# Kernel tuning notes

Measured on AMD Instinct MI355X. Metric: run time of the kernel, lower is better.

Reference implementation:

```python
import jax, jax.numpy as jnp
import numpy as np

B, T, D = 2, 2048, 2048
H = 16
HD = D // H  # 128


def _rotate_half(x):
    x1, x2 = x[..., :HD // 2], x[..., HD // 2:]
    return jnp.concatenate((-x2, x1), axis=-1)


def setup_inputs() -> dict:
    key = jax.random.key(0)
    ks = jax.random.split(key, 7)
    return {
        "x": jax.random.normal(ks[0], (B, T, D), dtype=jnp.float32),
        "rope_cos": jax.random.uniform(ks[1], (1, 1, T, HD), dtype=jnp.float32),
        "rope_sin": jax.random.uniform(ks[2], (1, 1, T, HD), dtype=jnp.float32),
        "qkv_w": jax.random.normal(ks[3], (3 * D, D), dtype=jnp.float32) * (1.0 / np.sqrt(D)),
        "qkv_b": jax.random.normal(ks[4], (3 * D,), dtype=jnp.float32) * 0.02,
        "out_w": jax.random.normal(ks[5], (D, D), dtype=jnp.float32) * (1.0 / np.sqrt(D)),
        "out_b": jax.random.normal(ks[6], (D,), dtype=jnp.float32) * 0.02,
    }


def reference(x, rope_cos, rope_sin, qkv_w, qkv_b, out_w, out_b):
    bsz, t, d = x.shape
    # fused QKV projection (torch Linear: x @ W.T + b)
    qkv = x @ qkv_w.T + qkv_b                       # [B, T, 3D]
    qkv = qkv.reshape(bsz, t, 3, H, HD).transpose(2, 0, 3, 1, 4)  # [3, B, H, T, HD]
    q, k, v = qkv[0], qkv[1], qkv[2]
    # RoPE
    cos = rope_cos[:, :, :t, :]
    sin = rope_sin[:, :, :t, :]
    q = q * cos + _rotate_half(q) * sin
    k = k * cos + _rotate_half(k) * sin
    # causal SDPA (eval mode -> no dropout)
    scale = 1.0 / np.sqrt(HD)
    scores = jnp.einsum("bhqd,bhkd->bhqk", q, k) * scale
    causal = jnp.tril(jnp.ones((t, t), dtype=bool))
    scores = jnp.where(causal, scores, jnp.finfo(scores.dtype).min)
    attn = jax.nn.softmax(scores, axis=-1)
    out = jnp.einsum("bhqk,bhkd->bhqd", attn, v)    # [B, H, T, HD]
    out = out.transpose(0, 2, 1, 3).reshape(bsz, t, d)
    return out @ out_w.T + out_b
```

## Files before the change

### kernel.cpp

```cpp
#include <hip/hip_runtime.h>

typedef unsigned short u16;
typedef __attribute__((ext_vector_type(8))) short bf16x8;
typedef __attribute__((ext_vector_type(4))) float f32x4;

__device__ __forceinline__ float bf2f(unsigned int u) {
    union { unsigned int i; float f; } x; x.i = u << 16; return x.f;
}
__device__ __forceinline__ u16 f2bf(float f) {
    union { float f; unsigned int i; } x; x.f = f;
    unsigned int r = x.i + 0x7fffu + ((x.i >> 16) & 1u);
    return (u16)(r >> 16);
}

__device__ __forceinline__ void gl2lds16(const u16* g, u16* l) {
    __builtin_amdgcn_global_load_lds(
        (const __attribute__((address_space(1))) unsigned int*)g,
        (__attribute__((address_space(3))) unsigned int*)l, 16, 0, 0);
}

#define NX  8388608
#define NW1 12582912
#define NW2 4194304
__global__ __launch_bounds__(256) void convert_kernel(
    const float* __restrict__ x, const float* __restrict__ w1,
    const float* __restrict__ w2, u16* __restrict__ dst)
{
    const int i = (blockIdx.x * 256 + threadIdx.x) * 4;
    const float* src;
    int off;
    if (i < NX)            { src = x;  off = i; }
    else if (i < NX + NW1) { src = w1; off = i - NX; }
    else                   { src = w2; off = i - NX - NW1; }
    float4 v = *(const float4*)(src + off);
    ushort4 o;
    o.x = f2bf(v.x); o.y = f2bf(v.y); o.z = f2bf(v.z); o.w = f2bf(v.w);
    *(ushort4*)(dst + i) = o;
}

#define NTILES 64
#define BUFSZ  12288

#define GEMM_SETUP(Ag, Bg)                                                    \
    const int tid = threadIdx.x;                                              \
    const int wave = tid >> 6, lane = tid & 63;                               \
    const int l16 = lane & 15, quad = lane >> 4;                              \
    const int wr = wave >> 2, wc = wave & 3;                                  \
    f32x4 acc[4][4];                                                          \
    _Pragma("unroll") for (int mi = 0; mi < 4; ++mi)                          \
        _Pragma("unroll") for (int ni = 0; ni < 4; ++ni)                      \
            acc[mi][ni] = (f32x4){0.f, 0.f, 0.f, 0.f};                        \
    int aoff[4], boff[4];                                                     \
    _Pragma("unroll") for (int mi = 0; mi < 4; ++mi) {                        \
        const int r = wr * 64 + mi * 16 + l16;                                \
        aoff[mi] = r * 32 + ((quad ^ ((r >> 1) & 3)) << 3);                   \
    }                                                                         \
    _Pragma("unroll") for (int ni = 0; ni < 4; ++ni) {                        \
        const int r = (wc >> 1) * 128 + (ni >> 1) * 64 + (wc & 1) * 32        \
                    + (ni & 1) * 16 + l16;                                    \
        boff[ni] = 4096 + r * 32 + ((quad ^ ((r >> 1) & 3)) << 3);            \
    }                                                                         \
    const u16* sbase[3]; int sdst[3];                                         \
    _Pragma("unroll") for (int j = 0; j < 3; ++j) {                           \
        const int c = wave * 3 + j;                                           \
        const int g = lane & 3;                                               \
        int r; const u16* bp; int d;                                          \
        if (c < 8) {                                                          \
            r = c * 16 + (lane >> 2);                                         \
            bp = Ag + (size_t)(m0 + r) * 2048;                                \
            d = c * 512 + lane * 8;                                           \
        } else {                                                              \
            r = (c - 8) * 16 + (lane >> 2);                                   \
            bp = Bg + (size_t)(n0 + r) * 2048;                                \
            d = 4096 + (c - 8) * 512 + lane * 8;                              \
        }                                                                     \
        sbase[j] = bp + ((g ^ ((r >> 1) & 3)) << 3);                          \
        sdst[j] = d;                                                          \
    }                                                                         \
         \
    _Pragma("unroll") for (int pt = 0; pt < 2; ++pt)                          \
        _Pragma("unroll") for (int j = 0; j < 3; ++j)                         \
            gl2lds16(sbase[j] + pt * 32, lds + pt * BUFSZ + sdst[j]);         \
    bf16x8 afr[2][4], bfr[2][4];                                              \
    asm volatile("s_waitcnt vmcnt(3)" ::: "memory");                          \
    __builtin_amdgcn_s_barrier();                                             \
    _Pragma("unroll") for (int mi = 0; mi < 4; ++mi)                          \
        afr[0][mi] = *(const bf16x8*)(lds + aoff[mi]);                        \
    _Pragma("unroll") for (int ni = 0; ni < 4; ++ni)                          \
        bfr[0][ni] = *(const bf16x8*)(lds + boff[ni]);

#define GPH(TT, SS, RS, PAR, STG, VMN, RD, LGN)                               \
    {                                                                         \
        if (STG) {                                                            \
            u16* nb = lds + (SS) * BUFSZ;                                     \
            _Pragma("unroll") for (int j = 0; j < 3; ++j)                     \
                gl2lds16(sbase[j] + ((TT) + 2) * 32, nb + sdst[j]);           \
        }                                                                     \
        asm volatile("s_waitcnt vmcnt(" #VMN ")" ::: "memory");               \
        __builtin_amdgcn_s_barrier();                                         \
        if (RD) {                                                             \
            const u16* rb = lds + (RS) * BUFSZ;                               \
            _Pragma("unroll") for (int mi = 0; mi < 4; ++mi)                  \
                afr[(PAR) ^ 1][mi] = *(const bf16x8*)(rb + aoff[mi]);         \
            _Pragma("unroll") for (int ni = 0; ni < 4; ++ni)                  \
                bfr[(PAR) ^ 1][ni] = *(const bf16x8*)(rb + boff[ni]);         \
        }                                                                     \
        asm volatile("s_waitcnt lgkmcnt(" #LGN ")" ::: "memory");             \
        __builtin_amdgcn_sched_barrier(0);                                    \
        __builtin_amdgcn_s_setprio(1);                                        \
        _Pragma("unroll") for (int mi = 0; mi < 4; ++mi)                      \
            _Pragma("unroll") for (int ni = 0; ni < 4; ++ni)                  \
                acc[mi][ni] = __builtin_amdgcn_mfma_f32_16x16x32_bf16(        \
                    afr[PAR][mi], bfr[PAR][ni], acc[mi][ni], 0, 0, 0);        \
        __builtin_amdgcn_s_setprio(0);                                        \
        __builtin_amdgcn_sched_barrier(0);                                    \
        __builtin_amdgcn_s_barrier();                                         \
    }

#define GEMM_MAIN()                                                           \
    for (int t = 0; t < 10; ++t) {                                            \
        const int T = t * 6;                                                  \
        GPH(T,     2, 1, 0, 1, 3, 1, 8)                                       \
        GPH(T + 1, 0, 2, 1, 1, 3, 1, 8)                                       \
        GPH(T + 2, 1, 0, 0, 1, 3, 1, 8)                                       \
        GPH(T + 3, 2, 1, 1, 1, 3, 1, 8)                                       \
        GPH(T + 4, 0, 2, 0, 1, 3, 1, 8)                                       \
        GPH(T + 5, 1, 0, 1, 1, 3, 1, 8)                                       \
    }                                                                         \
    GPH(60, 2, 1, 0, 1, 3, 1, 8)                                              \
    GPH(61, 0, 2, 1, 1, 3, 1, 8)                                              \
    GPH(62, 1, 0, 0, 0, 0, 1, 8)                                              \
    GPH(63, 2, 1, 1, 0, 0, 0, 0)

__global__ __launch_bounds__(512, 2) void qkv8_kernel(
    const u16* __restrict__ xb, const u16* __restrict__ wb,
    const float* __restrict__ bias, const float* __restrict__ rc,
    const float* __restrict__ rs, u16* __restrict__ Qo,
    u16* __restrict__ Ko, u16* __restrict__ Vo)
{
    __shared__ u16 lds[3 * BUFSZ];
    const int bid = blockIdx.x;
    const int xcd = bid & 7, j = bid >> 3;
    const int m0 = (xcd * 4 + (j & 3)) * 128;
    const int n0 = (j >> 2) * 256;

    GEMM_SETUP(xb, wb)
    GEMM_MAIN()

    const int e  = n0 >> 11;
    const int h  = ((n0 & 2047) >> 7) + (wc >> 1);
    const int hb = n0 + (wc >> 1) * 128;
    const int hq = wc & 1;
    if (e < 2) {
        u16* dst = (e == 0) ? Qo : Ko;
        #pragma unroll
        for (int mi = 0; mi < 4; ++mi) {
            #pragma unroll
            for (int r = 0; r < 4; ++r) {
                const int m = m0 + wr * 64 + mi * 16 + quad * 4 + r;
                const int b = m >> 11, tt = m & 2047;
                u16* drow = dst + ((size_t)(b * 16 + h) * 2048 + tt) * 128;
                const float* crow = rc + tt * 128;
                const float* sr2  = rs + tt * 128;
                #pragma unroll
                for (int p = 0; p < 2; ++p) {
                    const int hd1 = hq * 32 + p * 16 + l16;
                    const int hd2 = hd1 + 64;
                    const float v1 = acc[mi][p][r]     + bias[hb + hd1];
                    const float v2 = acc[mi][p + 2][r] + bias[hb + hd2];
                    drow[hd1] = f2bf(v1 * crow[hd1] - v2 * sr2[hd1]);
                    drow[hd2] = f2bf(v2 * crow[hd2] + v1 * sr2[hd2]);
                }
            }
        }
    } else {
        #pragma unroll
        for (int mi = 0; mi < 4; ++mi) {
            const int mb = m0 + wr * 64 + mi * 16 + quad * 4;
            const int b = mb >> 11, tt = mb & 2047;
            u16* vbase = Vo + (size_t)(b * 16 + h) * 128 * 2048 + tt;
            #pragma unroll
            for (int ni = 0; ni < 4; ++ni) {
                const int hd = (ni >> 1) * 64 + hq * 32 + (ni & 1) * 16 + l16;
                const float bs = bias[hb + hd];
                ushort4 o;
                #pragma unroll
                for (int r = 0; r < 4; ++r)
                    ((u16*)&o)[r] = f2bf(acc[mi][ni][r] + bs);
                *(ushort4*)(vbase + (size_t)hd * 2048) = o;
            }
        }
    }
}

#define KPAD 136
#define VPAD 72
#define PPAD 72

__global__ __launch_bounds__(256) void attn_mfma_kernel(
    const u16* __restrict__ Qi, const u16* __restrict__ Ki,
    const u16* __restrict__ Vg, u16* __restrict__ Oo)
{
    __shared__ u16 Ks[64 * KPAD];
    __shared__ u16 Vt[128 * VPAD];
    __shared__ u16 Ps[4][16 * PPAD];

    const int tid  = threadIdx.x;
    const int wave = tid >> 6, lane = tid & 63;
    const int l16 = lane & 15, quad = lane >> 4;
    const int bh = blockIdx.y;
    const size_t base = (size_t)bh * (2048 * 128);

    const int qtile[2] = { (int)blockIdx.x, 31 - (int)blockIdx.x };

    bf16x8 qf[2][4];
    f32x4 o[2][8];
    float l_i[2][4];
    #pragma unroll
    for (int s = 0; s < 2; ++s) {
        const u16* qp = Qi + base + (size_t)(qtile[s] * 64 + wave * 16 + l16) * 128 + quad * 8;
        #pragma unroll
        for (int c = 0; c < 4; ++c) qf[s][c] = *(const bf16x8*)(qp + c * 32);
        #pragma unroll
        for (int i = 0; i < 8; ++i) o[s][i] = (f32x4){0.f, 0.f, 0.f, 0.f};
        #pragma unroll
        for (int r = 0; r < 4; ++r) l_i[s][r] = 0.f;
    }

    const float scale = 0.08838834764831845f;
    const int ntiles = qtile[1] + 1;

    for (int t = 0; t < ntiles; ++t) {
        const int kt = t * 64;
        __syncthreads();
        {
            const int key = tid >> 2, d0 = (tid & 3) * 32;
            const u16* src = Ki + base + (size_t)(kt + key) * 128 + d0;
            u16* dst = Ks + key * KPAD + d0;
            #pragma unroll
            for (int i = 0; i < 4; ++i)
                *(bf16x8*)(dst + 8 * i) = *(const bf16x8*)(src + 8 * i);
        }
        {
            const int d = tid >> 1, koff = (tid & 1) * 32;
            const u16* src = Vg + ((size_t)bh * 128 + d) * 2048 + kt + koff;
            u16* dst = Vt + d * VPAD + koff;
            #pragma unroll
            for (int i = 0; i < 4; ++i)
                *(bf16x8*)(dst + 8 * i) = *(const bf16x8*)(src + 8 * i);
        }
        __syncthreads();

        const bool act_a = (t <= qtile[0]);

        f32x4 sa[4], sb[4];
        #pragma unroll
        for (int nt = 0; nt < 4; ++nt) {
            sa[nt] = (f32x4){0.f, 0.f, 0.f, 0.f};
            sb[nt] = (f32x4){0.f, 0.f, 0.f, 0.f};
            #pragma unroll
            for (int c = 0; c < 4; ++c) {
                bf16x8 kf = *(const bf16x8*)(Ks + (nt * 16 + l16) * KPAD + c * 32 + quad * 8);
                sb[nt] = __builtin_amdgcn_mfma_f32_16x16x32_bf16(qf[1][c], kf, sb[nt], 0, 0, 0);
                sa[nt] = __builtin_amdgcn_mfma_f32_16x16x32_bf16(qf[0][c], kf, sa[nt], 0, 0, 0);
            }
        }

        #pragma unroll
        for (int s = 0; s < 2; ++s) {
            if (s == 0 && !act_a) continue;
            f32x4* sc = (s == 0) ? sa : sb;
            const int qrow = qtile[s] * 64 + wave * 16 + quad * 4;
            const bool diag = (t == qtile[s]);

            #pragma unroll
            for (int nt = 0; nt < 4; ++nt) {
                #pragma unroll
                for (int r = 0; r < 4; ++r) {
                    float v = sc[nt][r] * scale - 11.0f;
                    if (diag) {
                        const int key = kt + nt * 16 + l16;
                        v = (key <= qrow + r) ? v : -1.0e30f;
                    }
                    const float e = __expf(v);
                    sc[nt][r] = e;
                    l_i[s][r] += e;
                }
            }

            u16* pw = Ps[wave];
            #pragma unroll
            for (int nt = 0; nt < 4; ++nt)
                #pragma unroll
                for (int r = 0; r < 4; ++r)
                    pw[(quad * 4 + r) * PPAD + nt * 16 + l16] = f2bf(sc[nt][r]);

            bf16x8 pf0 = *(const bf16x8*)(pw + l16 * PPAD + quad * 8);
            bf16x8 pf1 = *(const bf16x8*)(pw + l16 * PPAD + 32 + quad * 8);

            #pragma unroll
            for (int nt = 0; nt < 8; ++nt) {
                bf16x8 vf0 = *(const bf16x8*)(Vt + (nt * 16 + l16) * VPAD + quad * 8);
                bf16x8 vf1 = *(const bf16x8*)(Vt + (nt * 16 + l16) * VPAD + 32 + quad * 8);
                o[s][nt] = __builtin_amdgcn_mfma_f32_16x16x32_bf16(pf0, vf0, o[s][nt], 0, 0, 0);
                o[s][nt] = __builtin_amdgcn_mfma_f32_16x16x32_bf16(pf1, vf1, o[s][nt], 0, 0, 0);
            }
        }
    }

    const int b = bh >> 4, h = bh & 15;
    #pragma unroll
    for (int s = 0; s < 2; ++s) {
        const int qrow = qtile[s] * 64 + wave * 16 + quad * 4;
        #pragma unroll
        for (int r = 0; r < 4; ++r) {
            float ls = l_i[s][r];
            ls += __shfl_xor(ls, 1, 16);
            ls += __shfl_xor(ls, 2, 16);
            ls += __shfl_xor(ls, 4, 16);
            ls += __shfl_xor(ls, 8, 16);
            const float inv = 1.f / ls;
            u16* orow = Oo + ((size_t)(b * 2048 + qrow + r)) * 2048 + h * 128 + l16;
            #pragma unroll
            for (int nt = 0; nt < 8; ++nt)
                orow[nt * 16] = f2bf(o[s][nt][r] * inv);
        }
    }
}

__global__ __launch_bounds__(512, 2) void proj8_kernel(
    const u16* __restrict__ A, const u16* __restrict__ wb,
    const float* __restrict__ bias, float* __restrict__ out)
{
    __shared__ u16 lds[3 * BUFSZ];
    const int bid = blockIdx.x;
    const int xcd = bid & 7, j = bid >> 3;
    const int m0 = (xcd * 4 + (j & 3)) * 128;
    const int n0 = (j >> 2) * 256;

    GEMM_SETUP(A, wb)
    GEMM_MAIN()

    #pragma unroll
    for (int mi = 0; mi < 4; ++mi) {
        #pragma unroll
        for (int r = 0; r < 4; ++r) {
            const int m = m0 + wr * 64 + mi * 16 + quad * 4 + r;
            float* orow = out + (size_t)m * 2048;
            #pragma unroll
            for (int ni = 0; ni < 4; ++ni) {
                const int n = n0 + (wc >> 1) * 128 + (ni >> 1) * 64
                            + (wc & 1) * 32 + (ni & 1) * 16 + l16;
                orow[n] = acc[mi][ni][r] + bias[n];
            }
        }
    }
}

extern "C" void kernel_launch(void* const* d_in, const int* in_sizes, int n_in,
                              void* d_out, int out_size, void* d_ws, size_t ws_size,
                              hipStream_t stream) {
    const float* x     = (const float*)d_in[0];
    const float* rcos  = (const float*)d_in[1];
    const float* rsin  = (const float*)d_in[2];
    const float* qkv_w = (const float*)d_in[3];
    const float* qkv_b = (const float*)d_in[4];
    const float* out_w = (const float*)d_in[5];
    const float* out_b = (const float*)d_in[6];
    float* out = (float*)d_out;

    const size_t NE = (size_t)2 * 16 * 2048 * 128;
    u16* Q      = (u16*)d_ws;
    u16* K      = Q + NE;
    u16* V      = K + NE;
    u16* xb     = V + NE;
    u16* O      = xb;
    u16* qkv_wb = xb + NX;
    u16* out_wb = qkv_wb + NW1;

    convert_kernel<<<dim3((NX + NW1 + NW2) / 1024), 256, 0, stream>>>(
        x, qkv_w, out_w, xb);
    qkv8_kernel<<<dim3(768), 512, 0, stream>>>(
        xb, qkv_wb, qkv_b, rcos, rsin, Q, K, V);
    attn_mfma_kernel<<<dim3(16, 32), 256, 0, stream>>>(Q, K, V, O);
    proj8_kernel<<<dim3(256), 512, 0, stream>>>(O, out_wb, out_b, out);
}
```

Measured before the change: 380.8 us.

## Restructure GEMM pipeline to four LDS buffers with two k-tiles per barrier

The GEMM main loop used by the QKV and output projection kernels now runs on a 4-stage LDS ring instead of 3. It prefetches two k-tiles per super-step and computes two k-tiles between barriers, with LDS fragment reads interleaved between the MFMA groups. This halves the number of workgroup barriers and vmcnt waits per k-loop and deepens the prefetch distance. In exchange it uses more LDS per block, which may limit the two-blocks-per-CU occupancy, and it adds a full lgkmcnt(0) drain each step.

```diff
diff --git a/kernel.cpp b/kernel.cpp
--- a/kernel.cpp
+++ b/kernel.cpp
@@ -77,60 +77,81 @@
         sbase[j] = bp + ((g ^ ((r >> 1) & 3)) << 3);                          \
         sdst[j] = d;                                                          \
     }                                                                         \
-         \
-    _Pragma("unroll") for (int pt = 0; pt < 2; ++pt)                          \
+       \
+    _Pragma("unroll") for (int pt = 0; pt < 4; ++pt)                          \
         _Pragma("unroll") for (int j = 0; j < 3; ++j)                         \
             gl2lds16(sbase[j] + pt * 32, lds + pt * BUFSZ + sdst[j]);         \
     bf16x8 afr[2][4], bfr[2][4];                                              \
-    asm volatile("s_waitcnt vmcnt(3)" ::: "memory");                          \
+    asm volatile("s_waitcnt vmcnt(6)" ::: "memory");                          \
     __builtin_amdgcn_s_barrier();                                             \
     _Pragma("unroll") for (int mi = 0; mi < 4; ++mi)                          \
         afr[0][mi] = *(const bf16x8*)(lds + aoff[mi]);                        \
     _Pragma("unroll") for (int ni = 0; ni < 4; ++ni)                          \
-        bfr[0][ni] = *(const bf16x8*)(lds + boff[ni]);
-
-#define GPH(TT, SS, RS, PAR, STG, VMN, RD, LGN)                               \
+        bfr[0][ni] = *(const bf16x8*)(lds + boff[ni]);                        \
+    _Pragma("unroll") for (int mi = 0; mi < 4; ++mi)                          \
+        afr[1][mi] = *(const bf16x8*)(lds + BUFSZ + aoff[mi]);                \
+    _Pragma("unroll") for (int ni = 0; ni < 4; ++ni)                          \
+        bfr[1][ni] = *(const bf16x8*)(lds + BUFSZ + boff[ni]);                \
+    asm volatile("s_waitcnt lgkmcnt(0)" ::: "memory");                        \
+    __builtin_amdgcn_sched_barrier(0);                                        \
+    __builtin_amdgcn_s_barrier();
+
+#define SUP(TT, A0, A1, A2, A3, STG, VMN, RD)                                 \
     {                                                                         \
         if (STG) {                                                            \
-            u16* nb = lds + (SS) * BUFSZ;                                     \
-            _Pragma("unroll") for (int j = 0; j < 3; ++j)                     \
-                gl2lds16(sbase[j] + ((TT) + 2) * 32, nb + sdst[j]);           \
+            u16* nb0 = lds + (A0) * BUFSZ;                                    \
+            u16* nb1 = lds + (A1) * BUFSZ;                                    \
+            _Pragma("unroll") for (int j = 0; j < 3; ++j) {                   \
+                gl2lds16(sbase[j] + ((TT) + 4) * 32, nb0 + sdst[j]);          \
+                gl2lds16(sbase[j] + ((TT) + 5) * 32, nb1 + sdst[j]);          \
+            }                                                                 \
         }                                                                     \
         asm volatile("s_waitcnt vmcnt(" #VMN ")" ::: "memory");               \
+        __builtin_amdgcn_sched_barrier(0);                                    \
         __builtin_amdgcn_s_barrier();                                         \
-        if (RD) {                                                             \
-            const u16* rb = lds + (RS) * BUFSZ;                               \
-            _Pragma("unroll") for (int mi = 0; mi < 4; ++mi)                  \
-                afr[(PAR) ^ 1][mi] = *(const bf16x8*)(rb + aoff[mi]);         \
-            _Pragma("unroll") for (int ni = 0; ni < 4; ++ni)                  \
-                bfr[(PAR) ^ 1][ni] = *(const bf16x8*)(rb + boff[ni]);         \
-        }                                                                     \
-        asm volatile("s_waitcnt lgkmcnt(" #LGN ")" ::: "memory");             \
         __builtin_amdgcn_sched_barrier(0);                                    \
         __builtin_amdgcn_s_setprio(1);                                        \
         _Pragma("unroll") for (int mi = 0; mi < 4; ++mi)                      \
             _Pragma("unroll") for (int ni = 0; ni < 4; ++ni)                  \
                 acc[mi][ni] = __builtin_amdgcn_mfma_f32_16x16x32_bf16(        \
-                    afr[PAR][mi], bfr[PAR][ni], acc[mi][ni], 0, 0, 0);        \
+                    afr[0][mi], bfr[0][ni], acc[mi][ni], 0, 0, 0);            \
         __builtin_amdgcn_s_setprio(0);                                        \
         __builtin_amdgcn_sched_barrier(0);                                    \
+        if (RD) {                                                             \
+            const u16* rb = lds + (A2) * BUFSZ;                               \
+            _Pragma("unroll") for (int mi = 0; mi < 4; ++mi)                  \
+                afr[0][mi] = *(const bf16x8*)(rb + aoff[mi]);                 \
+            _Pragma("unroll") for (int ni = 0; ni < 4; ++ni)                  \
+                bfr[0][ni] = *(const bf16x8*)(rb + boff[ni]);                 \
+        }                                                                     \
+        __builtin_amdgcn_sched_barrier(0);                                    \
+        __builtin_amdgcn_s_setprio(1);                                        \
+        _Pragma("unroll") for (int mi = 0; mi < 4; ++mi)                      \
+            _Pragma("unroll") for (int ni = 0; ni < 4; ++ni)                  \
+                acc[mi][ni] = __builtin_amdgcn_mfma_f32_16x16x32_bf16(        \
+                    afr[1][mi], bfr[1][ni], acc[mi][ni], 0, 0, 0);            \
+        __builtin_amdgcn_s_setprio(0);                                        \
+        __builtin_amdgcn_sched_barrier(0);                                    \
+        if (RD) {                                                             \
+            const u16* rb2 = lds + (A3) * BUFSZ;                              \
+            _Pragma("unroll") for (int mi = 0; mi < 4; ++mi)                  \
+                afr[1][mi] = *(const bf16x8*)(rb2 + aoff[mi]);                \
+            _Pragma("unroll") for (int ni = 0; ni < 4; ++ni)                  \
+                bfr[1][ni] = *(const bf16x8*)(rb2 + boff[ni]);                \
+        }                                                                     \
+        asm volatile("s_waitcnt lgkmcnt(0)" ::: "memory");                    \
+        __builtin_amdgcn_sched_barrier(0);                                    \
         __builtin_amdgcn_s_barrier();                                         \
     }
 
 #define GEMM_MAIN()                                                           \
-    for (int t = 0; t < 10; ++t) {                                            \
-        const int T = t * 6;                                                  \
-        GPH(T,     2, 1, 0, 1, 3, 1, 8)                                       \
-        GPH(T + 1, 0, 2, 1, 1, 3, 1, 8)                                       \
-        GPH(T + 2, 1, 0, 0, 1, 3, 1, 8)                                       \
-        GPH(T + 3, 2, 1, 1, 1, 3, 1, 8)                                       \
-        GPH(T + 4, 0, 2, 0, 1, 3, 1, 8)                                       \
-        GPH(T + 5, 1, 0, 1, 1, 3, 1, 8)                                       \
+    for (int s = 0; s < 15; ++s) {                                            \
+        const int T = s * 4;                                                  \
+        SUP(T,     0, 1, 2, 3, 1, 6, 1)                                       \
+        SUP(T + 2, 2, 3, 0, 1, 1, 6, 1)                                       \
     }                                                                         \
-    GPH(60, 2, 1, 0, 1, 3, 1, 8)                                              \
-    GPH(61, 0, 2, 1, 1, 3, 1, 8)                                              \
-    GPH(62, 1, 0, 0, 0, 0, 1, 8)                                              \
-    GPH(63, 2, 1, 1, 0, 0, 0, 0)
+    SUP(60, 0, 1, 2, 3, 0, 0, 1)                                              \
+    SUP(62, 2, 3, 0, 1, 0, 0, 0)
 
 __global__ __launch_bounds__(512, 2) void qkv8_kernel(
     const u16* __restrict__ xb, const u16* __restrict__ wb,
@@ -138,7 +159,7 @@
     const float* __restrict__ rs, u16* __restrict__ Qo,
     u16* __restrict__ Ko, u16* __restrict__ Vo)
 {
-    __shared__ u16 lds[3 * BUFSZ];
+    __shared__ u16 lds[4 * BUFSZ];
     const int bid = blockIdx.x;
     const int xcd = bid & 7, j = bid >> 3;
     const int m0 = (xcd * 4 + (j & 3)) * 128;
@@ -332,7 +353,7 @@
     const u16* __restrict__ A, const u16* __restrict__ wb,
     const float* __restrict__ bias, float* __restrict__ out)
 {
-    __shared__ u16 lds[3 * BUFSZ];
+    __shared__ u16 lds[4 * BUFSZ];
     const int bid = blockIdx.x;
     const int xcd = bid & 7, j = bid >> 3;
     const int m0 = (xcd * 4 + (j & 3)) * 128;
```

Result: no change. 379.1 us (-0.5%).
